# Performance work log

Hardware: AMD Instinct MI355X
Metric: run time of the kernel (lower is better)

Reference implementation:

```python
import jax, jax.numpy as jnp
import numpy as np

B, H, W = 16, 1024, 1024
BOUNDARY_WEIGHT = 2.0
FOCAL_ALPHA = 0.25
FOCAL_GAMMA = 2.0
SMOOTH = 1e-6


def setup_inputs() -> dict:
    key = jax.random.key(0)
    k1, k2, k3 = jax.random.split(key, 3)
    pred_masks = jax.random.normal(k1, (B, 1, H, W), dtype=jnp.float32)
    gt_masks = jax.random.bernoulli(k2, 0.5, (B, 1, H, W)).astype(jnp.float32)
    pred_iou = jax.random.uniform(k3, (B, 1), dtype=jnp.float32)
    return {"pred_masks": pred_masks, "gt_masks": gt_masks, "pred_iou": pred_iou}


def _bce_with_logits(x, t):
    # stable: softplus(x) - x*t == -[t*log(sig(x)) + (1-t)*log(1-sig(x))]
    return jax.nn.softplus(x) - x * t


def reference(pred_masks, gt_masks, pred_iou):
    x, t = pred_masks, gt_masks
    ce = _bce_with_logits(x, t)                      # (B,1,H,W)
    p = jax.nn.sigmoid(x)

    # focal loss
    p_t = p * t + (1.0 - p) * (1.0 - t)
    alpha_t = FOCAL_ALPHA * t + (1.0 - FOCAL_ALPHA) * (1.0 - t)
    focal = jnp.mean(alpha_t * ce * (1.0 - p_t) ** FOCAL_GAMMA)

    # dice loss
    intersection = jnp.sum(p * t, axis=(2, 3))       # (B,1)
    union = jnp.sum(p, axis=(2, 3)) + jnp.sum(t, axis=(2, 3))
    dice = 1.0 - jnp.mean((2.0 * intersection + SMOOTH) / (union + SMOOTH))

    # boundary-weighted BCE. In the source, dist = EDT(mask) is 0 at every
    # background pixel and dist_inv = EDT(1-mask) is 0 at every foreground
    # pixel, so min(dist, dist_inv) == 0 <= 3 at EVERY pixel -> the weight
    # map is uniformly boundary_weight. Faithful equivalent:
    boundary = BOUNDARY_WEIGHT * jnp.mean(ce)

    total = focal + dice + 0.5 * boundary

    # IoU auxiliary loss (thresholded prediction; no grad flows through >0.5)
    pred_bin = (p > 0.5).astype(x.dtype)
    inter = jnp.sum(pred_bin * t, axis=(1, 2, 3))    # (B,)
    uni = jnp.sum(pred_bin, axis=(1, 2, 3)) + jnp.sum(t, axis=(1, 2, 3)) - inter
    actual_iou = (inter + SMOOTH) / (uni + SMOOTH)
    iou_loss = jnp.mean((jnp.squeeze(pred_iou) - actual_iou) ** 2)

    return total + 0.1 * iou_loss
```

## Files before the change

### kernel.cpp

```cpp
#include <hip/hip_runtime.h>
#include <math.h>


#define HW_PIX (1024 * 1024)
#define BATCH 16
constexpr int BLOCKS_PER_IMG = 256;
constexpr int THREADS = 256;
constexpr int PIX_PER_BLOCK = HW_PIX / BLOCKS_PER_IMG;
constexpr int ITERS = PIX_PER_BLOCK / (THREADS * 4);

__global__ __launch_bounds__(THREADS) void
loss_partial(const float* __restrict__ x, const float* __restrict__ t,
             float* __restrict__ acc) {
  const int b = blockIdx.x / BLOCKS_PER_IMG;
  const int chunk = blockIdx.x % BLOCKS_PER_IMG;
  const long base = (long)b * HW_PIX + (long)chunk * PIX_PER_BLOCK;
  const float4* __restrict__ x4 = (const float4*)(x + base);
  const float4* __restrict__ t4 = (const float4*)(t + base);

  float4 xv[ITERS], tv[ITERS];
#pragma unroll
  for (int i = 0; i < ITERS; ++i) {
    xv[i] = x4[threadIdx.x + i * THREADS];
    tv[i] = t4[threadIdx.x + i * THREADS];
  }

  float fsum = 0.f, csum = 0.f, isum = 0.f, psum = 0.f;
  unsigned tcnt = 0, bicnt = 0, bpcnt = 0;

#pragma unroll
  for (int i = 0; i < ITERS; ++i) {
    const float* xs = reinterpret_cast<const float*>(&xv[i]);
    const float* ts = reinterpret_cast<const float*>(&tv[i]);
#pragma unroll
    for (int j = 0; j < 4; ++j) {
      const float xx = xs[j];
      const float tt = ts[j];
      const float e = __expf(-fabsf(xx));
      const float s = 1.0f + e;
      const float r = __builtin_amdgcn_rcpf(s);
      const float p = (xx >= 0.0f) ? r : e * r;
      const float ce = fmaxf(xx, 0.0f) - xx * tt + __logf(s);
      const float om = fmaf(tt, 1.0f - 2.0f * p, p);
      const float at = 0.75f - 0.5f * tt;
      fsum += at * ce * om * om;
      csum += ce;
      isum = fmaf(p, tt, isum);
      psum += p;
      const unsigned long long mt = __ballot(tt != 0.0f);
      const unsigned long long mb = __ballot(xx > 0.0f);
      tcnt  += (unsigned)__popcll(mt);
      bpcnt += (unsigned)__popcll(mb);
      bicnt += (unsigned)__popcll(mt & mb);
    }
  }

  __shared__ float red[THREADS / 64][7];
  const int lane = threadIdx.x & 63;
  const int wave = threadIdx.x >> 6;
  float vals[4] = {fsum, csum, isum, psum};
#pragma unroll
  for (int k = 0; k < 4; ++k) {
    float v = vals[k];
#pragma unroll
    for (int off = 32; off > 0; off >>= 1) v += __shfl_down(v, off);
    if (lane == 0) red[wave][k] = v;
  }
  if (lane == 0) {
    red[wave][4] = (float)tcnt;
    red[wave][5] = (float)bicnt;
    red[wave][6] = (float)bpcnt;
  }
  __syncthreads();
  if (threadIdx.x < 7) {
    const float s = red[0][threadIdx.x] + red[1][threadIdx.x] +
                    red[2][threadIdx.x] + red[3][threadIdx.x];
    atomicAdd(&acc[b * 7 + threadIdx.x], s);
  }
}

__global__ void loss_final(const float* __restrict__ acc,
                           const float* __restrict__ pred_iou,
                           float* __restrict__ out) {
  constexpr float SMOOTH = 1e-6f;
  const int lane = threadIdx.x;
  float F = 0.f, C = 0.f, D = 0.f, Q = 0.f;
  if (lane < BATCH) {
    const float* a = acc + lane * 7;
    F = a[0];
    C = a[1];
    const float I = a[2], P = a[3], T = a[4], BI = a[5], BP = a[6];
    D = (2.0f * I + SMOOTH) / (P + T + SMOOTH);
    const float iou = (BI + SMOOTH) / (BP + T - BI + SMOOTH);
    const float d = pred_iou[lane] - iou;
    Q = d * d;
  }
#pragma unroll
  for (int off = 32; off > 0; off >>= 1) {
    F += __shfl_down(F, off);
    C += __shfl_down(C, off);
    D += __shfl_down(D, off);
    Q += __shfl_down(Q, off);
  }
  if (lane == 0) {
    const float invN = 1.0f / (float)((long)BATCH * HW_PIX);
    const float focal = F * invN;
    const float dice = 1.0f - D * (1.0f / (float)BATCH);
    const float half_boundary = C * invN;
    const float iou_loss = Q * (1.0f / (float)BATCH);
    out[0] = focal + dice + half_boundary + 0.1f * iou_loss;
  }
}

extern "C" void kernel_launch(void* const* d_in, const int* in_sizes, int n_in,
                              void* d_out, int out_size, void* d_ws,
                              size_t ws_size, hipStream_t stream) {
  const float* x = (const float*)d_in[0];
  const float* t = (const float*)d_in[1];
  const float* piou = (const float*)d_in[2];
  float* acc = (float*)d_ws;

  hipMemsetAsync(acc, 0, BATCH * 7 * sizeof(float), stream);
  loss_partial<<<BATCH * BLOCKS_PER_IMG, THREADS, 0, stream>>>(x, t, acc);
  loss_final<<<1, 64, 0, stream>>>(acc, piou, (float*)d_out);
}
```

Baseline: 151.6 us.

## Stream inputs through per-wave LDS ring with async global-to-LDS loads

Replaces one-shot register loads with a persistent-style grid of 1024 blocks, each wave streaming its pixels through a 4-slot LDS ring filled by global_load_lds, using vmcnt waits to overlap loads with math. Per-block partials are written to a workspace instead of atomics, which removes the memset, and the final kernel reduces 64 partials per image. Adds manual waitcnt encoding and LDS round-trip cost. Per-wave in-flight depth may be lower than the old register prefetch.

```diff
diff --git a/kernel.cpp b/kernel.cpp
--- a/kernel.cpp
+++ b/kernel.cpp
@@ -4,43 +4,73 @@
 
 #define HW_PIX (1024 * 1024)
 #define BATCH 16
-constexpr int BLOCKS_PER_IMG = 256;
+constexpr int GRID = 1024;
+constexpr int BLOCKS_PER_IMG = GRID / BATCH;
 constexpr int THREADS = 256;
+constexpr int WAVES = THREADS / 64;
 constexpr int PIX_PER_BLOCK = HW_PIX / BLOCKS_PER_IMG;
-constexpr int ITERS = PIX_PER_BLOCK / (THREADS * 4);
+constexpr int PIX_PER_WAVE = PIX_PER_BLOCK / WAVES;
+constexpr int SLOT_PX = 256;
+constexpr int NSLOT = PIX_PER_WAVE / SLOT_PX;
+constexpr int RING = 4;
+constexpr int SLOT_BYTES = SLOT_PX * 4;
+constexpr int WAVE_LDS = RING * 2 * SLOT_BYTES;
+
+typedef const __attribute__((address_space(1))) unsigned int* gas_ptr;
+typedef __attribute__((address_space(3))) unsigned int* las_ptr;
+
+#define WAIT_VM6() { __builtin_amdgcn_s_waitcnt(0xF76); asm volatile("" ::: "memory"); }
+#define WAIT_VM4() { __builtin_amdgcn_s_waitcnt(0xF74); asm volatile("" ::: "memory"); }
+#define WAIT_VM2() { __builtin_amdgcn_s_waitcnt(0xF72); asm volatile("" ::: "memory"); }
+#define WAIT_VM0() { __builtin_amdgcn_s_waitcnt(0xF70); asm volatile("" ::: "memory"); }
 
 __global__ __launch_bounds__(THREADS) void
 loss_partial(const float* __restrict__ x, const float* __restrict__ t,
              float* __restrict__ acc) {
+  __shared__ char smem[WAVES * WAVE_LDS];
+  __shared__ float red[WAVES][7];
+
   const int b = blockIdx.x / BLOCKS_PER_IMG;
   const int chunk = blockIdx.x % BLOCKS_PER_IMG;
-  const long base = (long)b * HW_PIX + (long)chunk * PIX_PER_BLOCK;
-  const float4* __restrict__ x4 = (const float4*)(x + base);
-  const float4* __restrict__ t4 = (const float4*)(t + base);
-
-  float4 xv[ITERS], tv[ITERS];
-#pragma unroll
-  for (int i = 0; i < ITERS; ++i) {
-    xv[i] = x4[threadIdx.x + i * THREADS];
-    tv[i] = t4[threadIdx.x + i * THREADS];
-  }
+  const int wave = threadIdx.x >> 6;
+  const int lane = threadIdx.x & 63;
+  const long wbase = (long)b * HW_PIX + (long)chunk * PIX_PER_BLOCK +
+                     (long)wave * PIX_PER_WAVE;
+  const float* gx = x + wbase;
+  const float* gt = t + wbase;
+  char* lds = smem + wave * WAVE_LDS;
 
   float fsum = 0.f, csum = 0.f, isum = 0.f, psum = 0.f;
   unsigned tcnt = 0, bicnt = 0, bpcnt = 0;
 
-#pragma unroll
-  for (int i = 0; i < ITERS; ++i) {
-    const float* xs = reinterpret_cast<const float*>(&xv[i]);
-    const float* ts = reinterpret_cast<const float*>(&tv[i]);
+  auto issue = [&](int slot) {
+    const int s = slot & (RING - 1);
+    const float* gxp = gx + slot * SLOT_PX + lane * 4;
+    const float* gtp = gt + slot * SLOT_PX + lane * 4;
+    char* lxp = lds + s * 2 * SLOT_BYTES;
+    char* ltp = lxp + SLOT_BYTES;
+    __builtin_amdgcn_global_load_lds((gas_ptr)(const void*)gxp,
+                                     (las_ptr)(void*)lxp, 16, 0, 0);
+    __builtin_amdgcn_global_load_lds((gas_ptr)(const void*)gtp,
+                                     (las_ptr)(void*)ltp, 16, 0, 0);
+  };
+
+  auto compute = [&](int slot) {
+    const int s = slot & (RING - 1);
+    const float4 xv = *(const float4*)(lds + s * 2 * SLOT_BYTES + lane * 16);
+    const float4 tv =
+        *(const float4*)(lds + s * 2 * SLOT_BYTES + SLOT_BYTES + lane * 16);
+    const float* xs = reinterpret_cast<const float*>(&xv);
+    const float* ts = reinterpret_cast<const float*>(&tv);
 #pragma unroll
     for (int j = 0; j < 4; ++j) {
       const float xx = xs[j];
       const float tt = ts[j];
       const float e = __expf(-fabsf(xx));
-      const float s = 1.0f + e;
-      const float r = __builtin_amdgcn_rcpf(s);
+      const float sp = 1.0f + e;
+      const float r = __builtin_amdgcn_rcpf(sp);
       const float p = (xx >= 0.0f) ? r : e * r;
-      const float ce = fmaxf(xx, 0.0f) - xx * tt + __logf(s);
+      const float ce = fmaxf(xx, 0.0f) - xx * tt + __logf(sp);
       const float om = fmaf(tt, 1.0f - 2.0f * p, p);
       const float at = 0.75f - 0.5f * tt;
       fsum += at * ce * om * om;
@@ -49,15 +79,24 @@
       psum += p;
       const unsigned long long mt = __ballot(tt != 0.0f);
       const unsigned long long mb = __ballot(xx > 0.0f);
-      tcnt  += (unsigned)__popcll(mt);
+      tcnt += (unsigned)__popcll(mt);
       bpcnt += (unsigned)__popcll(mb);
       bicnt += (unsigned)__popcll(mt & mb);
     }
+  };
+
+  issue(0); issue(1); issue(2); issue(3);
+#pragma unroll
+  for (int j = 0; j < NSLOT - RING; ++j) {
+    WAIT_VM6();
+    compute(j);
+    issue(j + RING);
   }
+  WAIT_VM6(); compute(NSLOT - 4);
+  WAIT_VM4(); compute(NSLOT - 3);
+  WAIT_VM2(); compute(NSLOT - 2);
+  WAIT_VM0(); compute(NSLOT - 1);
 
-  __shared__ float red[THREADS / 64][7];
-  const int lane = threadIdx.x & 63;
-  const int wave = threadIdx.x >> 6;
   float vals[4] = {fsum, csum, isum, psum};
 #pragma unroll
   for (int k = 0; k < 4; ++k) {
@@ -73,9 +112,9 @@
   }
   __syncthreads();
   if (threadIdx.x < 7) {
-    const float s = red[0][threadIdx.x] + red[1][threadIdx.x] +
-                    red[2][threadIdx.x] + red[3][threadIdx.x];
-    atomicAdd(&acc[b * 7 + threadIdx.x], s);
+    acc[blockIdx.x * 7 + threadIdx.x] =
+        red[0][threadIdx.x] + red[1][threadIdx.x] +
+        red[2][threadIdx.x] + red[3][threadIdx.x];
   }
 }
 
@@ -83,32 +122,44 @@
                            const float* __restrict__ pred_iou,
                            float* __restrict__ out) {
   constexpr float SMOOTH = 1e-6f;
-  const int lane = threadIdx.x;
-  float F = 0.f, C = 0.f, D = 0.f, Q = 0.f;
-  if (lane < BATCH) {
-    const float* a = acc + lane * 7;
-    F = a[0];
-    C = a[1];
-    const float I = a[2], P = a[3], T = a[4], BI = a[5], BP = a[6];
-    D = (2.0f * I + SMOOTH) / (P + T + SMOOTH);
-    const float iou = (BI + SMOOTH) / (BP + T - BI + SMOOTH);
-    const float d = pred_iou[lane] - iou;
-    Q = d * d;
+  __shared__ float fin[BATCH][7];
+  const int tid = threadIdx.x;
+  if (tid < BATCH * 7) {
+    const int b = tid / 7, k = tid % 7;
+    float s = 0.f;
+    for (int i = 0; i < BLOCKS_PER_IMG; ++i)
+      s += acc[(b * BLOCKS_PER_IMG + i) * 7 + k];
+    fin[b][k] = s;
   }
+  __syncthreads();
+  if (tid < 64) {
+    const int lane = tid;
+    float F = 0.f, C = 0.f, D = 0.f, Q = 0.f;
+    if (lane < BATCH) {
+      F = fin[lane][0];
+      C = fin[lane][1];
+      const float I = fin[lane][2], P = fin[lane][3], T = fin[lane][4],
+                  BI = fin[lane][5], BP = fin[lane][6];
+      D = (2.0f * I + SMOOTH) / (P + T + SMOOTH);
+      const float iou = (BI + SMOOTH) / (BP + T - BI + SMOOTH);
+      const float d = pred_iou[lane] - iou;
+      Q = d * d;
+    }
 #pragma unroll
-  for (int off = 32; off > 0; off >>= 1) {
-    F += __shfl_down(F, off);
-    C += __shfl_down(C, off);
-    D += __shfl_down(D, off);
-    Q += __shfl_down(Q, off);
-  }
-  if (lane == 0) {
-    const float invN = 1.0f / (float)((long)BATCH * HW_PIX);
-    const float focal = F * invN;
-    const float dice = 1.0f - D * (1.0f / (float)BATCH);
-    const float half_boundary = C * invN;
-    const float iou_loss = Q * (1.0f / (float)BATCH);
-    out[0] = focal + dice + half_boundary + 0.1f * iou_loss;
+    for (int off = 32; off > 0; off >>= 1) {
+      F += __shfl_down(F, off);
+      C += __shfl_down(C, off);
+      D += __shfl_down(D, off);
+      Q += __shfl_down(Q, off);
+    }
+    if (lane == 0) {
+      const float invN = 1.0f / (float)((long)BATCH * HW_PIX);
+      const float focal = F * invN;
+      const float dice = 1.0f - D * (1.0f / (float)BATCH);
+      const float half_boundary = C * invN;
+      const float iou_loss = Q * (1.0f / (float)BATCH);
+      out[0] = focal + dice + half_boundary + 0.1f * iou_loss;
+    }
   }
 }
 
@@ -120,7 +171,6 @@
   const float* piou = (const float*)d_in[2];
   float* acc = (float*)d_ws;
 
-  hipMemsetAsync(acc, 0, BATCH * 7 * sizeof(float), stream);
-  loss_partial<<<BATCH * BLOCKS_PER_IMG, THREADS, 0, stream>>>(x, t, acc);
-  loss_final<<<1, 64, 0, stream>>>(acc, piou, (float*)d_out);
+  loss_partial<<<GRID, THREADS, 0, stream>>>(x, t, acc);
+  loss_final<<<1, 128, 0, stream>>>(acc, piou, (float*)d_out);
 }
```

Result: slower. 157.3 us (+3.8%).

## Stride loads across blocks and replace atomics with per-block partials plus final reduce

Applied to the files above, without the earlier changes.

Each block now reads pixels with a grid-wide stride pattern inside its image instead of a contiguous chunk, and loads are issued inside the loop instead of all being prefetched into registers up front. The per-batch atomicAdd accumulation and the memset are replaced by per-block partial stores, which the final kernel sums serially (112 threads each looping over 256 partials). This removes the memset launch and the atomic contention. In exchange, prefetch depth may drop and the final kernel gains a serial reduction.

```diff
diff --git a/kernel.cpp b/kernel.cpp
--- a/kernel.cpp
+++ b/kernel.cpp
@@ -4,43 +4,38 @@
 
 #define HW_PIX (1024 * 1024)
 #define BATCH 16
-constexpr int BLOCKS_PER_IMG = 256;
+constexpr int BPI = 256;
+constexpr int GRID = BATCH * BPI;
 constexpr int THREADS = 256;
-constexpr int PIX_PER_BLOCK = HW_PIX / BLOCKS_PER_IMG;
-constexpr int ITERS = PIX_PER_BLOCK / (THREADS * 4);
+constexpr int STRIDE_PX = BPI * THREADS * 4;
+constexpr int ITERS = HW_PIX / STRIDE_PX;
 
 __global__ __launch_bounds__(THREADS) void
 loss_partial(const float* __restrict__ x, const float* __restrict__ t,
              float* __restrict__ acc) {
-  const int b = blockIdx.x / BLOCKS_PER_IMG;
-  const int chunk = blockIdx.x % BLOCKS_PER_IMG;
-  const long base = (long)b * HW_PIX + (long)chunk * PIX_PER_BLOCK;
-  const float4* __restrict__ x4 = (const float4*)(x + base);
-  const float4* __restrict__ t4 = (const float4*)(t + base);
-
-  float4 xv[ITERS], tv[ITERS];
-#pragma unroll
-  for (int i = 0; i < ITERS; ++i) {
-    xv[i] = x4[threadIdx.x + i * THREADS];
-    tv[i] = t4[threadIdx.x + i * THREADS];
-  }
+  const int b = blockIdx.x >> 8;
+  const int chunk = blockIdx.x & (BPI - 1);
+  const long base =
+      (long)b * HW_PIX + ((long)chunk * THREADS + threadIdx.x) * 4;
 
   float fsum = 0.f, csum = 0.f, isum = 0.f, psum = 0.f;
   unsigned tcnt = 0, bicnt = 0, bpcnt = 0;
 
 #pragma unroll
   for (int i = 0; i < ITERS; ++i) {
-    const float* xs = reinterpret_cast<const float*>(&xv[i]);
-    const float* ts = reinterpret_cast<const float*>(&tv[i]);
+    const float4 xv = *(const float4*)(x + base + (long)i * STRIDE_PX);
+    const float4 tv = *(const float4*)(t + base + (long)i * STRIDE_PX);
+    const float* xs = reinterpret_cast<const float*>(&xv);
+    const float* ts = reinterpret_cast<const float*>(&tv);
 #pragma unroll
     for (int j = 0; j < 4; ++j) {
       const float xx = xs[j];
       const float tt = ts[j];
       const float e = __expf(-fabsf(xx));
-      const float s = 1.0f + e;
-      const float r = __builtin_amdgcn_rcpf(s);
+      const float sp = 1.0f + e;
+      const float r = __builtin_amdgcn_rcpf(sp);
       const float p = (xx >= 0.0f) ? r : e * r;
-      const float ce = fmaxf(xx, 0.0f) - xx * tt + __logf(s);
+      const float ce = fmaxf(xx, 0.0f) - xx * tt + __logf(sp);
       const float om = fmaf(tt, 1.0f - 2.0f * p, p);
       const float at = 0.75f - 0.5f * tt;
       fsum += at * ce * om * om;
@@ -49,7 +44,7 @@
       psum += p;
       const unsigned long long mt = __ballot(tt != 0.0f);
       const unsigned long long mb = __ballot(xx > 0.0f);
-      tcnt  += (unsigned)__popcll(mt);
+      tcnt += (unsigned)__popcll(mt);
       bpcnt += (unsigned)__popcll(mb);
       bicnt += (unsigned)__popcll(mt & mb);
     }
@@ -73,9 +68,9 @@
   }
   __syncthreads();
   if (threadIdx.x < 7) {
-    const float s = red[0][threadIdx.x] + red[1][threadIdx.x] +
-                    red[2][threadIdx.x] + red[3][threadIdx.x];
-    atomicAdd(&acc[b * 7 + threadIdx.x], s);
+    acc[blockIdx.x * 7 + threadIdx.x] =
+        red[0][threadIdx.x] + red[1][threadIdx.x] +
+        red[2][threadIdx.x] + red[3][threadIdx.x];
   }
 }
 
@@ -83,32 +78,44 @@
                            const float* __restrict__ pred_iou,
                            float* __restrict__ out) {
   constexpr float SMOOTH = 1e-6f;
-  const int lane = threadIdx.x;
-  float F = 0.f, C = 0.f, D = 0.f, Q = 0.f;
-  if (lane < BATCH) {
-    const float* a = acc + lane * 7;
-    F = a[0];
-    C = a[1];
-    const float I = a[2], P = a[3], T = a[4], BI = a[5], BP = a[6];
-    D = (2.0f * I + SMOOTH) / (P + T + SMOOTH);
-    const float iou = (BI + SMOOTH) / (BP + T - BI + SMOOTH);
-    const float d = pred_iou[lane] - iou;
-    Q = d * d;
+  __shared__ float fin[BATCH][7];
+  const int tid = threadIdx.x;
+  if (tid < BATCH * 7) {
+    const int b = tid / 7, k = tid % 7;
+    float s = 0.f;
+    for (int i = 0; i < BPI; ++i)
+      s += acc[(b * BPI + i) * 7 + k];
+    fin[b][k] = s;
   }
+  __syncthreads();
+  if (tid < 64) {
+    const int lane = tid;
+    float F = 0.f, C = 0.f, D = 0.f, Q = 0.f;
+    if (lane < BATCH) {
+      F = fin[lane][0];
+      C = fin[lane][1];
+      const float I = fin[lane][2], P = fin[lane][3], T = fin[lane][4],
+                  BI = fin[lane][5], BP = fin[lane][6];
+      D = (2.0f * I + SMOOTH) / (P + T + SMOOTH);
+      const float iou = (BI + SMOOTH) / (BP + T - BI + SMOOTH);
+      const float d = pred_iou[lane] - iou;
+      Q = d * d;
+    }
 #pragma unroll
-  for (int off = 32; off > 0; off >>= 1) {
-    F += __shfl_down(F, off);
-    C += __shfl_down(C, off);
-    D += __shfl_down(D, off);
-    Q += __shfl_down(Q, off);
-  }
-  if (lane == 0) {
-    const float invN = 1.0f / (float)((long)BATCH * HW_PIX);
-    const float focal = F * invN;
-    const float dice = 1.0f - D * (1.0f / (float)BATCH);
-    const float half_boundary = C * invN;
-    const float iou_loss = Q * (1.0f / (float)BATCH);
-    out[0] = focal + dice + half_boundary + 0.1f * iou_loss;
+    for (int off = 32; off > 0; off >>= 1) {
+      F += __shfl_down(F, off);
+      C += __shfl_down(C, off);
+      D += __shfl_down(D, off);
+      Q += __shfl_down(Q, off);
+    }
+    if (lane == 0) {
+      const float invN = 1.0f / (float)((long)BATCH * HW_PIX);
+      const float focal = F * invN;
+      const float dice = 1.0f - D * (1.0f / (float)BATCH);
+      const float half_boundary = C * invN;
+      const float iou_loss = Q * (1.0f / (float)BATCH);
+      out[0] = focal + dice + half_boundary + 0.1f * iou_loss;
+    }
   }
 }
 
@@ -120,7 +127,6 @@
   const float* piou = (const float*)d_in[2];
   float* acc = (float*)d_ws;
 
-  hipMemsetAsync(acc, 0, BATCH * 7 * sizeof(float), stream);
-  loss_partial<<<BATCH * BLOCKS_PER_IMG, THREADS, 0, stream>>>(x, t, acc);
-  loss_final<<<1, 64, 0, stream>>>(acc, piou, (float*)d_out);
+  loss_partial<<<GRID, THREADS, 0, stream>>>(x, t, acc);
+  loss_final<<<1, 128, 0, stream>>>(acc, piou, (float*)d_out);
 }
```

After: 157.8 us. +4.1%, slower.
